# Performance work log

Hardware: AMD Instinct MI355X
Metric: run time of the kernel (lower is better)

## Reference

```python
import jax, jax.numpy as jnp
import numpy as np
from jax import lax

SOBEL_X = jnp.array([[-1., 0., 1.], [-2., 0., 2.], [-1., 0., 1.]], jnp.float32)
SCHARR_X = jnp.array([[-3., 0., 3.], [-10., 0., 10.], [-3., 0., 3.]], jnp.float32)

# year routing map baked in (configure()): 2019->sobel(0), 2020->scharr(1), default learnable(2)

def _dwconv(x, k2d):
    """Depthwise 3x3 conv with the same 2D kernel per channel, padding=1."""
    C = x.shape[1]
    kern = jnp.broadcast_to(k2d, (C, 1, 3, 3))
    return lax.conv_general_dilated(
        x, kern, window_strides=(1, 1), padding='SAME',
        dimension_numbers=('NCHW', 'OIHW', 'NCHW'), feature_group_count=C)


def _edge_mag(x, kx, ky, eps):
    gx = _dwconv(x, kx)
    gy = _dwconv(x, ky)
    return jnp.sqrt(gx * gx + gy * gy + eps)


def setup_inputs() -> dict:
    key = jax.random.key(0)
    k1, k2 = jax.random.split(key)
    x = jax.random.normal(k1, (32, 9, 256, 256), jnp.float32)
    year = 2018 + jax.random.randint(k2, (32,), 0, 4)  # years 2018..2021
    alpha = jnp.asarray(0.5, jnp.float32)
    scale = jnp.ones((1,), jnp.float32) * 0.1
    return {"x": x, "alpha": alpha, "scale": scale, "year": year}


def reference(x, alpha, scale, year):
    B = x.shape[0]
    # fixed operators
    sobel_out = _edge_mag(x, SOBEL_X, SOBEL_X.T, 1e-8)
    scharr_out = _edge_mag(x, SCHARR_X, SCHARR_X.T, 1e-8)
    # learnable operator: sigmoid-mixed kernel, normalized by max abs
    a = jax.nn.sigmoid(alpha)
    kx = a * SOBEL_X + (1.0 - a) * SCHARR_X
    kx = kx / jnp.max(jnp.abs(kx))
    ky = kx.T  # sobel_y = sobel_x.T and scharr_y = scharr_x.T, mix commutes with transpose
    learnable_out = _edge_mag(x, kx, ky, 1e-6) * jax.nn.sigmoid(scale)
    # per-sample routing: 2019 -> sobel, 2020 -> scharr, else default learnable
    op_idx = jnp.where(year == 2019, 0, jnp.where(year == 2020, 1, 2))
    stacked = jnp.stack([sobel_out, scharr_out, learnable_out])  # [3,B,C,H,W]
    mixed = stacked[op_idx, jnp.arange(B)]
    return mixed
```

## Files before the change

kernel.cpp:

```cpp
#include <hip/hip_runtime.h>
#include <math.h>

#define BATCH 32
#define CHANS 9
#define HH 256
#define WW 256

typedef float f32x4 __attribute__((ext_vector_type(4)));

__global__ __launch_bounds__(256) void edge_router_kernel(
    const float* __restrict__ x,
    const float* __restrict__ alpha_p,
    const float* __restrict__ scale_p,
    const int*   __restrict__ year,
    float* __restrict__ out)
{
    const int bid   = blockIdx.x;
    const int strip = bid & 7;
    const int plane = bid >> 3;
    const int b     = plane / CHANS;

    const int tid  = threadIdx.x;
    const int wave = tid >> 6;
    const int lane = tid & 63;

    const int y0 = strip * 32 + wave * 8;
    const int xq = lane * 4;

    const float* __restrict__ p = x   + (size_t)plane * (HH * WW);
    float*       __restrict__ q = out + (size_t)plane * (HH * WW);

    const int yr = year[b];
    float w0, w1, eps, post;
    if (yr == 2019) {
        w0 = 1.f; w1 = 2.f; eps = 1e-8f; post = 1.f;
    } else if (yr == 2020) {
        w0 = 3.f; w1 = 10.f; eps = 1e-8f; post = 1.f;
    } else {
        const float a = 1.f / (1.f + expf(-alpha_p[0]));
        const float m = 10.f - 8.f * a;
        w0 = (3.f - 2.f * a) / m;
        w1 = 1.f;
        eps = 1e-6f;
        post = 1.f / (1.f + expf(-scale_p[0]));
    }

    f32x4 v[10];
    #pragma unroll
    for (int i = 0; i < 10; ++i) {
        int y  = y0 - 1 + i;
        int yc = min(max(y, 0), HH - 1);
        v[i] = *reinterpret_cast<const f32x4*>(p + (size_t)yc * WW + xq);
    }
    if (y0 == 0)       v[0] = (f32x4)0.f;
    if (y0 + 8 == HH)  v[9] = (f32x4)0.f;

    auto derive = [&](f32x4 vv, f32x4& d, f32x4& s) {
        float left  = __shfl_up(vv.w, 1);
        if (lane == 0)  left  = 0.f;
        float right = __shfl_down(vv.x, 1);
        if (lane == 63) right = 0.f;
        d.x = vv.y - left;  d.y = vv.z - vv.x;
        d.z = vv.w - vv.y;  d.w = right - vv.z;
        s.x = fmaf(w1, vv.x, w0 * (left + vv.y));
        s.y = fmaf(w1, vv.y, w0 * (vv.x + vv.z));
        s.z = fmaf(w1, vv.z, w0 * (vv.y + vv.w));
        s.w = fmaf(w1, vv.w, w0 * (vv.z + right));
    };

    f32x4 dm, sm, d0, s0v;
    derive(v[0], dm, sm);
    derive(v[1], d0, s0v);

    #pragma unroll
    for (int r = 0; r < 8; ++r) {
        f32x4 dp, sp;
        derive(v[r + 2], dp, sp);

        f32x4 o;
        {
            float gx = fmaf(w1, d0.x, w0 * (dm.x + dp.x));
            float gy = sp.x - sm.x;
            o.x = sqrtf(fmaf(gx, gx, fmaf(gy, gy, eps))) * post;
        }
        {
            float gx = fmaf(w1, d0.y, w0 * (dm.y + dp.y));
            float gy = sp.y - sm.y;
            o.y = sqrtf(fmaf(gx, gx, fmaf(gy, gy, eps))) * post;
        }
        {
            float gx = fmaf(w1, d0.z, w0 * (dm.z + dp.z));
            float gy = sp.z - sm.z;
            o.z = sqrtf(fmaf(gx, gx, fmaf(gy, gy, eps))) * post;
        }
        {
            float gx = fmaf(w1, d0.w, w0 * (dm.w + dp.w));
            float gy = sp.w - sm.w;
            o.w = sqrtf(fmaf(gx, gx, fmaf(gy, gy, eps))) * post;
        }

        __builtin_nontemporal_store(o, reinterpret_cast<f32x4*>(q + (size_t)(y0 + r) * WW + xq));

        dm = d0; sm = s0v;
        d0 = dp; s0v = sp;
    }
}

extern "C" void kernel_launch(void* const* d_in, const int* in_sizes, int n_in,
                              void* d_out, int out_size, void* d_ws, size_t ws_size,
                              hipStream_t stream) {
    const float* x     = (const float*)d_in[0];
    const float* alpha = (const float*)d_in[1];
    const float* scale = (const float*)d_in[2];
    const int*   year  = (const int*)  d_in[3];
    float* out = (float*)d_out;

    const int blocks = BATCH * CHANS * (HH / 32);
    edge_router_kernel<<<blocks, 256, 0, stream>>>(x, alpha, scale, year, out);
}
```

Before: 136.8 us.

## Assign one output row per wavefront instead of eight-row strips

Each wavefront now computes a single output row from three input rows, and the grid grows eightfold to cover every row. Before, a wave loaded ten rows and reused the horizontal derivatives across eight outputs. The goal is more parallelism and lower register pressure, but every input row is now read three times (mostly served from cache), shuffle and derive work roughly triples, and more blocks must be launched. The nontemporal store is also swapped for a plain store.

```diff
diff --git a/kernel.cpp b/kernel.cpp
--- a/kernel.cpp
+++ b/kernel.cpp
@@ -15,20 +15,24 @@
     const int*   __restrict__ year,
     float* __restrict__ out)
 {
-    const int bid   = blockIdx.x;
-    const int strip = bid & 7;
-    const int plane = bid >> 3;
+    const int tid   = threadIdx.x;
+    const int lane  = tid & 63;
+    const int gwave = blockIdx.x * 4 + (tid >> 6);
+    const int row   = gwave & (HH - 1);
+    const int plane = gwave >> 8;
     const int b     = plane / CHANS;
-
-    const int tid  = threadIdx.x;
-    const int wave = tid >> 6;
-    const int lane = tid & 63;
-
-    const int y0 = strip * 32 + wave * 8;
-    const int xq = lane * 4;
+    const int xq    = lane * 4;
 
     const float* __restrict__ p = x   + (size_t)plane * (HH * WW);
     float*       __restrict__ q = out + (size_t)plane * (HH * WW);
+
+    const int ym = row > 0 ? row - 1 : 0;
+    const int yp = row < HH - 1 ? row + 1 : HH - 1;
+    f32x4 vm = *reinterpret_cast<const f32x4*>(p + (size_t)ym  * WW + xq);
+    f32x4 v0 = *reinterpret_cast<const f32x4*>(p + (size_t)row * WW + xq);
+    f32x4 vp = *reinterpret_cast<const f32x4*>(p + (size_t)yp  * WW + xq);
+    if (row == 0)      vm = (f32x4)0.f;
+    if (row == HH - 1) vp = (f32x4)0.f;
 
     const int yr = year[b];
     float w0, w1, eps, post;
@@ -45,16 +49,6 @@
         post = 1.f / (1.f + expf(-scale_p[0]));
     }
 
-    f32x4 v[10];
-    #pragma unroll
-    for (int i = 0; i < 10; ++i) {
-        int y  = y0 - 1 + i;
-        int yc = min(max(y, 0), HH - 1);
-        v[i] = *reinterpret_cast<const f32x4*>(p + (size_t)yc * WW + xq);
-    }
-    if (y0 == 0)       v[0] = (f32x4)0.f;
-    if (y0 + 8 == HH)  v[9] = (f32x4)0.f;
-
     auto derive = [&](f32x4 vv, f32x4& d, f32x4& s) {
         float left  = __shfl_up(vv.w, 1);
         if (lane == 0)  left  = 0.f;
@@ -68,42 +62,34 @@
         s.w = fmaf(w1, vv.w, w0 * (vv.z + right));
     };
 
-    f32x4 dm, sm, d0, s0v;
-    derive(v[0], dm, sm);
-    derive(v[1], d0, s0v);
+    f32x4 dm, sm, d0, s0v, dp, sp;
+    derive(vm, dm, sm);
+    derive(v0, d0, s0v);
+    derive(vp, dp, sp);
 
-    #pragma unroll
-    for (int r = 0; r < 8; ++r) {
-        f32x4 dp, sp;
-        derive(v[r + 2], dp, sp);
+    f32x4 o;
+    {
+        float gx = fmaf(w1, d0.x, w0 * (dm.x + dp.x));
+        float gy = sp.x - sm.x;
+        o.x = sqrtf(fmaf(gx, gx, fmaf(gy, gy, eps))) * post;
+    }
+    {
+        float gx = fmaf(w1, d0.y, w0 * (dm.y + dp.y));
+        float gy = sp.y - sm.y;
+        o.y = sqrtf(fmaf(gx, gx, fmaf(gy, gy, eps))) * post;
+    }
+    {
+        float gx = fmaf(w1, d0.z, w0 * (dm.z + dp.z));
+        float gy = sp.z - sm.z;
+        o.z = sqrtf(fmaf(gx, gx, fmaf(gy, gy, eps))) * post;
+    }
+    {
+        float gx = fmaf(w1, d0.w, w0 * (dm.w + dp.w));
+        float gy = sp.w - sm.w;
+        o.w = sqrtf(fmaf(gx, gx, fmaf(gy, gy, eps))) * post;
+    }
 
-        f32x4 o;
-        {
-            float gx = fmaf(w1, d0.x, w0 * (dm.x + dp.x));
-            float gy = sp.x - sm.x;
-            o.x = sqrtf(fmaf(gx, gx, fmaf(gy, gy, eps))) * post;
-        }
-        {
-            float gx = fmaf(w1, d0.y, w0 * (dm.y + dp.y));
-            float gy = sp.y - sm.y;
-            o.y = sqrtf(fmaf(gx, gx, fmaf(gy, gy, eps))) * post;
-        }
-        {
-            float gx = fmaf(w1, d0.z, w0 * (dm.z + dp.z));
-            float gy = sp.z - sm.z;
-            o.z = sqrtf(fmaf(gx, gx, fmaf(gy, gy, eps))) * post;
-        }
-        {
-            float gx = fmaf(w1, d0.w, w0 * (dm.w + dp.w));
-            float gy = sp.w - sm.w;
-            o.w = sqrtf(fmaf(gx, gx, fmaf(gy, gy, eps))) * post;
-        }
-
-        __builtin_nontemporal_store(o, reinterpret_cast<f32x4*>(q + (size_t)(y0 + r) * WW + xq));
-
-        dm = d0; sm = s0v;
-        d0 = dp; s0v = sp;
-    }
+    *reinterpret_cast<f32x4*>(q + (size_t)row * WW + xq) = o;
 }
 
 extern "C" void kernel_launch(void* const* d_in, const int* in_sizes, int n_in,
@@ -115,6 +101,7 @@
     const int*   year  = (const int*)  d_in[3];
     float* out = (float*)d_out;
 
-    const int blocks = BATCH * CHANS * (HH / 32);
+    const int rows   = BATCH * CHANS * HH;
+    const int blocks = rows / 4;
     edge_router_kernel<<<blocks, 256, 0, stream>>>(x, alpha, scale, year, out);
 }
```

New measurement: 133.8 us. 1.02x faster.
